# Kernel tuning notes

Hardware: AMD Instinct MI355X
Metric: run time of the kernel (lower is better)

## Reference

```python
import jax, jax.numpy as jnp
import numpy as np

NB = 8      # n_blocks
DIM = 256   # model dim (= context_len in source)
DI = 512    # dim_inner = dim * expand(2)
DCONV = 4   # depthwise conv kernel
NS = 16     # d_state
DTR = 16    # dt_rank = ceil(dim/16)
NE = 4      # experts
INNER = 512 # MoE FFN inner = dim * multi(2)
L = 8192    # sequence length
HOR = 32    # horizon
EPS = 1e-3


def setup_inputs() -> dict:
    key = jax.random.key(0)
    ks = jax.random.split(key, 16)
    s = 0.02
    f = lambda k, shp: jax.random.normal(k, shp, jnp.float32) * s
    return {
        "x": jax.random.normal(ks[0], (DIM, L), jnp.float32),
        "lin_w": f(ks[1], (DIM, DIM)),                      # shared by self.linear and self.out (tied)
        "in_proj_w": f(ks[2], (NB, 2 * DI, DIM)),
        "conv_w": f(ks[3], (NB, DI, 1, DCONV)),             # depthwise conv, groups=DI
        "conv_b": f(ks[4], (NB, DI)),
        "x_proj_w": f(ks[5], (NB, DTR + 2 * NS, DI)),
        "dt_proj_w": f(ks[6], (NB, DI, DTR)),
        "dt_proj_b": f(ks[7], (NB, DI)),
        "A_log": jnp.tile(jnp.log(jnp.arange(1, NS + 1, dtype=jnp.float32)), (NB, DI, 1)),
        "D_param": jnp.ones((NB, DI), jnp.float32),
        "out_proj_w": f(ks[8], (NB, DIM, DI)),
        "gate_w": f(ks[9], (NB, NE, DIM)),
        "gproj_w": f(ks[10], (NB, NE, INNER, DIM)),
        "uproj_w": f(ks[11], (NB, NE, INNER, DIM)),
        "dproj_w": f(ks[12], (NB, NE, DIM, INNER)),
        "rms_a_w": jnp.ones((DIM,), jnp.float32),
        "rms_f_w": jnp.ones((DIM,), jnp.float32),
        "head_w1": f(ks[13], (DIM, DIM)),
        "head_w2": f(ks[14], (HOR, DIM)),
    }


def _rmsnorm(h, w):
    return w * (h * jax.lax.rsqrt(jnp.mean(h * h, axis=-1, keepdims=True) + EPS))


def _mamba(h, ipw, cw, cb, xpw, dtw, dtb, alog, dpar, opw):
    b = h.shape[0]
    xr = jnp.einsum('bld,od->bol', h, ipw)            # (b, 2*DI, l)
    xc, res = jnp.split(xr, 2, axis=1)                # each (b, DI, l)
    # causal depthwise conv (padding=DCONV-1, sliced to length l)
    xc = jax.lax.conv_general_dilated(xc, cw, (1,), [(DCONV - 1, 0)],
                                      feature_group_count=DI,
                                      dimension_numbers=('NCH', 'OIH', 'NCH'))
    xc = jax.nn.silu(xc + cb[None, :, None])
    A = -jnp.exp(alog)                                # (DI, NS)
    xdbl = jnp.einsum('bdl,kd->blk', xc, xpw)         # (b, l, DTR+2*NS)
    dr, B, C = xdbl[..., :DTR], xdbl[..., DTR:DTR + NS], xdbl[..., DTR + NS:]
    delta = jax.nn.softplus(jnp.einsum('blr,dr->bld', dr, dtw) + dtb)
    dA = jnp.exp(jnp.einsum('bld,dn->lbdn', delta, A))          # (l, b, DI, NS)
    dBu = jnp.einsum('bld,bln,bdl->lbdn', delta, B, xc)         # (l, b, DI, NS)
    Cl = jnp.transpose(C, (1, 0, 2))                             # (l, b, NS)
    def step(carry, inp):
        a, bu, c = inp
        carry = a * carry + bu
        return carry, jnp.einsum('bdn,bn->bd', carry, c)
    _, ys = jax.lax.scan(step, jnp.zeros((b, DI, NS), xc.dtype), (dA, dBu, Cl))
    y = jnp.transpose(ys, (1, 2, 0)) + xc * dpar[:, None]        # (b, DI, l)
    y = y * jax.nn.silu(res)
    return jnp.einsum('bdl,od->blo', y, opw)                     # (b, l, DIM)


def _moe(h, gw, gp, up, dp):
    shp = h.shape
    xf = h.reshape(-1, shp[-1])                       # (T, DIM)
    scores = xf @ gw.T                                # (T, NE)
    vals, idx = jax.lax.top_k(scores, 2)
    w = jax.nn.softmax(vals, axis=-1)                 # (T, 2)
    g = jax.nn.silu(jnp.einsum('td,ehd->teh', xf, gp))
    u = jnp.einsum('td,ehd->teh', xf, up)
    eo = jnp.einsum('teh,edh->ted', g * u, dp)        # (T, NE, DIM)
    we = jnp.sum(w[..., None] * jax.nn.one_hot(idx, NE, dtype=xf.dtype), axis=1)  # (T, NE)
    return jnp.einsum('te,ted->td', we, eo).reshape(shp)


def reference(x, lin_w, in_proj_w, conv_w, conv_b, x_proj_w, dt_proj_w, dt_proj_b,
              A_log, D_param, out_proj_w, gate_w, gproj_w, uproj_w, dproj_w,
              rms_a_w, rms_f_w, head_w1, head_w2):
    h = x.T[None]                                     # (1, L, DIM)
    h = h @ lin_w.T
    for i in range(NB):
        resi = h
        h = _rmsnorm(h, rms_a_w)
        h = _mamba(h, in_proj_w[i], conv_w[i], conv_b[i], x_proj_w[i],
                   dt_proj_w[i], dt_proj_b[i], A_log[i], D_param[i], out_proj_w[i])
        h = h + resi
        resi = h
        h = _moe(h, gate_w[i], gproj_w[i], uproj_w[i], dproj_w[i])
        h = _rmsnorm(h, rms_f_w)
        h = h + resi
    h = h @ lin_w.T                                   # self.out (tied weight)
    h = jax.nn.silu(h @ head_w1.T) @ head_w2.T        # head
    return jax.nn.sigmoid(h[0].T)                     # (HOR, L)
```

## Files before the change

### kernel.cpp

```cpp
#include <hip/hip_runtime.h>

typedef unsigned short u16;
typedef unsigned int u32;
using bf16x8 = __attribute__((ext_vector_type(8))) short;
using f32x4 = __attribute__((ext_vector_type(4))) float;

constexpr int kL = 8192;
constexpr int kDIM = 256;
constexpr int kDI = 512;
constexpr int kNB = 8;
constexpr float kEPS = 1e-3f;

__device__ __forceinline__ u16 f2b(float f) {
  u32 x = __builtin_bit_cast(u32, f);
  x += 0x7fffu + ((x >> 16) & 1u);
  return (u16)(x >> 16);
}
__device__ __forceinline__ float b2f(u16 u) {
  return __builtin_bit_cast(float, (u32)u << 16);
}
__device__ __forceinline__ float sigm(float x) { return 1.f / (1.f + __expf(-x)); }
__device__ __forceinline__ float softplus_fast(float x) {
  return fmaxf(x, 0.f) + __logf(1.f + __expf(-fabsf(x)));
}

__device__ __forceinline__ void async_cp16(const void* g, void* l) {
  __builtin_amdgcn_global_load_lds((const __attribute__((address_space(1))) u32*)g,
                                   (__attribute__((address_space(3))) u32*)l, 16, 0, 0);
}

struct Cvt2 {
  const float* s[23];
  u16* d[23];
  int n[23];
  int mode[23];
  int bstart[24];
  int nseg;
};
__global__ __launch_bounds__(256) void cvt2_k(Cvt2 dd) {
  const int b = blockIdx.x;
  int seg = 0;
  for (int i = 1; i < dd.nseg; ++i) seg += (b >= dd.bstart[i]) ? 1 : 0;
  const int lb = b - dd.bstart[seg];
  const float* s = dd.s[seg];
  u16* d = dd.d[seg];
  const int n = dd.n[seg];
  const int mode = dd.mode[seg];
  #pragma unroll
  for (int it = 0; it < 4; ++it) {
    const int e4 = lb * 1024 + it * 256 + threadIdx.x;
    const int i = e4 * 4;
    if (i >= n) break;
    const float4 v = ((const float4*)s)[e4];
    ushort4 o = make_ushort4(f2b(v.x), f2b(v.y), f2b(v.z), f2b(v.w));
    size_t dst;
    if (mode == 0) {
      dst = (size_t)i;
    } else if (mode == 1) {
      dst = (size_t)(((i >> 8) << 9) + (i & 255));
    } else {
      const int bb = i >> 19, e = (i >> 17) & 3, nr = (i >> 9) & 255, j = i & 511;
      dst = (size_t)bb * 524288 + (size_t)nr * 2048 + e * 512 + j;
    }
    *(ushort4*)&d[dst] = o;
  }
}

__global__ __launch_bounds__(256) void transpose_x_k(const float* __restrict__ x, u16* __restrict__ xT) {
  __shared__ float tile[32][33];
  int l0 = blockIdx.x * 32, d0 = blockIdx.y * 32;
  int tx = threadIdx.x, ty = threadIdx.y;
  #pragma unroll
  for (int i = 0; i < 32; i += 8)
    tile[ty + i][tx] = x[(size_t)(d0 + ty + i) * kL + l0 + tx];
  __syncthreads();
  #pragma unroll
  for (int i = 0; i < 32; i += 8)
    xT[(size_t)(l0 + ty + i) * kDIM + d0 + tx] = f2b(tile[tx][ty + i]);
}

template <int BM, int BN, int TR, int TC, int WCN, int MODE>
__global__ __launch_bounds__(256) void gemm_t(
    const u16* __restrict__ A, int lda,
    const u16* __restrict__ W, int ldw,
    void* __restrict__ C, int ldc,
    int N, int K, const float* __restrict__ wep, int pstride)
{
  constexpr int BNR = (BN + 63) & ~63;
  __shared__ u16 As[BM * 64];
  __shared__ u16 Bs[BNR * 64];
  const int tid = threadIdx.x;
  const int lane = tid & 63;
  const int wave = tid >> 6;
  const int bm = blockIdx.x * BM;
  const int bn = blockIdx.y * BN;
  const int wrow = (wave / WCN) * (TR * 16);
  const int wcol = (wave % WCN) * (TC * 16);
  const int kchunk = K / (int)gridDim.z;
  const int kbeg = blockIdx.z * kchunk;
  const int kend = kbeg + kchunk;

  f32x4 acc[TR][TC];
  #pragma unroll
  for (int r = 0; r < TR; ++r)
    #pragma unroll
    for (int c = 0; c < TC; ++c)
      acc[r][c] = f32x4{0.f, 0.f, 0.f, 0.f};

  for (int k0 = kbeg; k0 < kend; k0 += 64) {
    #pragma unroll
    for (int it = 0; it < BM * 64 / 2048; ++it) {
      int flat = (it * 256 + tid) * 8;
      int r = flat >> 6;
      int gc = ((((flat >> 3) & 7) ^ (r & 7)) << 3);
      async_cp16(A + (size_t)(bm + r) * lda + k0 + gc, &As[flat]);
    }
    #pragma unroll
    for (int it = 0; it < BNR * 64 / 2048; ++it) {
      int flat = (it * 256 + tid) * 8;
      int r = flat >> 6;
      int gc = ((((flat >> 3) & 7) ^ (r & 7)) << 3);
      int n = bn + r;
      if (n > N - 1) n = N - 1;
      async_cp16(W + (size_t)n * ldw + k0 + gc, &Bs[flat]);
    }
    __syncthreads();
    const int mrow = lane & 15;
    #pragma unroll
    for (int kk = 0; kk < 64; kk += 32) {
      const int kc = (kk >> 3) + (lane >> 4);
      bf16x8 a[TR], b[TC];
      #pragma unroll
      for (int rr = 0; rr < TR; ++rr) {
        int row = wrow + rr * 16 + mrow;
        a[rr] = *(const bf16x8*)&As[row * 64 + ((kc ^ (row & 7)) << 3)];
      }
      #pragma unroll
      for (int cc = 0; cc < TC; ++cc) {
        int row = wcol + cc * 16 + mrow;
        b[cc] = *(const bf16x8*)&Bs[row * 64 + ((kc ^ (row & 7)) << 3)];
      }
      #pragma unroll
      for (int rr = 0; rr < TR; ++rr)
        #pragma unroll
        for (int cc = 0; cc < TC; ++cc)
          acc[rr][cc] = __builtin_amdgcn_mfma_f32_16x16x32_bf16(a[rr], b[cc], acc[rr][cc], 0, 0, 0);
    }
    __syncthreads();
  }

  const int colb = bn + wcol + (lane & 15);
  const int rowb = bm + wrow + ((lane >> 4) << 2);
  if constexpr (MODE == 6) {
    #pragma unroll
    for (int rr = 0; rr < TR; ++rr)
      #pragma unroll
      for (int cc = 0; cc < TC; ++cc) {
        const int col = colb + cc * 16;
        #pragma unroll
        for (int i = 0; i < 4; ++i) {
          const float v = acc[rr][cc][i];
          const float partner = __shfl_xor(v, 1);
          if (!(lane & 1)) {
            const int row = rowb + rr * 16 + i;
            const int tsj = col >> 1;
            const float w = wep[row * 4 + (tsj >> 9)];
            ((u16*)C)[(size_t)row * 2048 + tsj] = f2b(v * sigm(v) * partner * w);
          }
        }
      }
  } else {
    #pragma unroll
    for (int rr = 0; rr < TR; ++rr)
      #pragma unroll
      for (int cc = 0; cc < TC; ++cc) {
        int col = colb + cc * 16;
        if (col >= N) continue;
        #pragma unroll
        for (int i = 0; i < 4; ++i) {
          const int row = rowb + rr * 16 + i;
          size_t off = (size_t)row * ldc + col;
          float v = acc[rr][cc][i];
          if constexpr (MODE == 0) ((float*)C)[off] = v;
          else if constexpr (MODE == 2) ((u16*)C)[off] = f2b(v);
          else if constexpr (MODE == 3) ((u16*)C)[off] = f2b(v * sigm(v));
          else if constexpr (MODE == 4) atomicAdd(&((float*)C)[off], v);
          else if constexpr (MODE == 5) ((float*)C)[off + (size_t)blockIdx.z * pstride] = v;
          else if constexpr (MODE == 7) ((float*)C)[(size_t)col * kL + row] = sigm(v);
        }
      }
  }
}

__device__ __forceinline__ float block_sum256(float v) {
  #pragma unroll
  for (int o = 32; o > 0; o >>= 1) v += __shfl_down(v, o);
  __shared__ float red[4];
  __syncthreads();
  if ((threadIdx.x & 63) == 0) red[threadIdx.x >> 6] = v;
  __syncthreads();
  return red[0] + red[1] + red[2] + red[3];
}

__global__ __launch_bounds__(256) void rms_a_k(const float* __restrict__ h, const float* __restrict__ w,
                                               u16* __restrict__ hn) {
  const int l = blockIdx.x, t = threadIdx.x;
  const float v = h[(size_t)l * kDIM + t];
  const float ssum = block_sum256(v * v);
  const float r = rsqrtf(ssum * (1.f / 256.f) + kEPS);
  hn[(size_t)l * kDIM + t] = f2b(w[t] * v * r);
}

__global__ __launch_bounds__(256) void rms_f_fused_k(const float* __restrict__ mpart,
                                                     const float* __restrict__ wf,
                                                     const float* __restrict__ wa,
                                                     float* __restrict__ h,
                                                     u16* __restrict__ hb2, u16* __restrict__ hn) {
  const int l = blockIdx.x, t = threadIdx.x;
  const size_t idx = (size_t)l * kDIM + t;
  const float m = mpart[idx] + mpart[idx + 2097152] + mpart[idx + 4194304] + mpart[idx + 6291456];
  const float r1 = rsqrtf(block_sum256(m * m) * (1.f / 256.f) + kEPS);
  const float hv = h[idx] + wf[t] * m * r1;
  h[idx] = hv;
  hb2[idx] = f2b(hv);
  const float r2 = rsqrtf(block_sum256(hv * hv) * (1.f / 256.f) + kEPS);
  hn[idx] = f2b(wa[t] * hv * r2);
}

__global__ __launch_bounds__(256) void conv_silu_k(const u16* __restrict__ xz, const float* __restrict__ cw,
                                                   const float* __restrict__ cb,
                                                   u16* __restrict__ xcb, u16* __restrict__ zsb,
                                                   float* __restrict__ xdbl) {
  const int i4 = blockIdx.x * 256 + threadIdx.x;
  if (i4 < 98304) *(float4*)&xdbl[i4 * 4] = float4{0.f, 0.f, 0.f, 0.f};
  const int l = i4 >> 7;
  const int d = (i4 & 127) * 4;
  float acc[4];
  const float4 cbv = *(const float4*)&cb[d];
  acc[0] = cbv.x; acc[1] = cbv.y; acc[2] = cbv.z; acc[3] = cbv.w;
  #pragma unroll
  for (int j = 0; j < 4; ++j) {
    const int ll = l - 3 + j;
    if (ll >= 0) {
      const ushort4 xv = *(const ushort4*)&xz[(size_t)ll * 1024 + d];
      acc[0] += cw[(d + 0) * 4 + j] * b2f(xv.x);
      acc[1] += cw[(d + 1) * 4 + j] * b2f(xv.y);
      acc[2] += cw[(d + 2) * 4 + j] * b2f(xv.z);
      acc[3] += cw[(d + 3) * 4 + j] * b2f(xv.w);
    }
  }
  ushort4 xo, zo;
  const ushort4 zv = *(const ushort4*)&xz[(size_t)l * 1024 + 512 + d];
  float z0 = b2f(zv.x), z1 = b2f(zv.y), z2 = b2f(zv.z), z3 = b2f(zv.w);
  xo.x = f2b(acc[0] * sigm(acc[0])); xo.y = f2b(acc[1] * sigm(acc[1]));
  xo.z = f2b(acc[2] * sigm(acc[2])); xo.w = f2b(acc[3] * sigm(acc[3]));
  zo.x = f2b(z0 * sigm(z0)); zo.y = f2b(z1 * sigm(z1));
  zo.z = f2b(z2 * sigm(z2)); zo.w = f2b(z3 * sigm(z3));
  *(ushort4*)&xcb[(size_t)l * 512 + d] = xo;
  *(ushort4*)&zsb[(size_t)l * 512 + d] = zo;
}

__global__ __launch_bounds__(256) void scan_a_k(const float* __restrict__ xdbl, const u16* __restrict__ xcb,
                                                const float* __restrict__ A_log, const float* __restrict__ dtw,
                                                const float* __restrict__ dtb,
                                                u16* __restrict__ delta,
                                                float* __restrict__ aprod, float* __restrict__ bacc) {
  const int c = blockIdx.x;
  const int t = threadIdx.x;
  const int half = t & 1;
  const int d = blockIdx.y * 128 + (t >> 1);
  const int l0 = c * 64;
  __shared__ float Xs[64][32];
  for (int i = t; i < 2048; i += 256)
    Xs[i >> 5][i & 31] = xdbl[(size_t)(l0 + (i >> 5)) * 48 + (i & 31)];
  __syncthreads();
  float wd[8], Ad[8];
  #pragma unroll
  for (int j = 0; j < 8; ++j) wd[j] = dtw[d * 16 + half * 8 + j];
  const float bd = dtb[d];
  #pragma unroll
  for (int n = 0; n < 8; ++n) Ad[n] = -__expf(A_log[d * 16 + half * 8 + n]);
  float s[8], ap[8];
  #pragma unroll
  for (int n = 0; n < 8; ++n) { s[n] = 0.f; ap[n] = 1.f; }
  #pragma unroll 4
  for (int lr = 0; lr < 64; ++lr) {
    const float4 dr0 = *(const float4*)&Xs[lr][half * 8];
    const float4 dr1 = *(const float4*)&Xs[lr][half * 8 + 4];
    float p0 = dr0.x * wd[0] + dr0.y * wd[1] + dr0.z * wd[2] + dr0.w * wd[3];
    float p1 = dr1.x * wd[4] + dr1.y * wd[5] + dr1.z * wd[6] + dr1.w * wd[7];
    float dot = p0 + p1;
    dot += __shfl_xor(dot, 1);
    const float dl = softplus_fast(dot + bd);
    const int l = l0 + lr;
    if (!half) delta[(size_t)l * 512 + d] = f2b(dl);
    const float du = dl * b2f(xcb[(size_t)l * 512 + d]);
    const float4 B0 = *(const float4*)&Xs[lr][16 + half * 8];
    const float4 B1 = *(const float4*)&Xs[lr][16 + half * 8 + 4];
    const float Bv[8] = {B0.x, B0.y, B0.z, B0.w, B1.x, B1.y, B1.z, B1.w};
    #pragma unroll
    for (int n = 0; n < 8; ++n) {
      const float a = __expf(dl * Ad[n]);
      s[n] = fmaf(a, s[n], du * Bv[n]);
      ap[n] *= a;
    }
  }
  const int base = c * 8192 + d * 16 + half * 8;
  #pragma unroll
  for (int n = 0; n < 8; ++n) { aprod[base + n] = ap[n]; bacc[base + n] = s[n]; }
}

__global__ __launch_bounds__(256) void scan_b_k(const float* __restrict__ aprod, const float* __restrict__ bacc,
                                                float* __restrict__ sinit) {
  const int st = blockIdx.x * 256 + threadIdx.x;
  float cur = 0.f;
  float a0 = aprod[st], b0 = bacc[st];
  for (int c = 0; c < 128; ++c) {
    float a1 = 0.f, b1 = 0.f;
    if (c + 1 < 128) {
      a1 = aprod[(size_t)(c + 1) * 8192 + st];
      b1 = bacc[(size_t)(c + 1) * 8192 + st];
    }
    sinit[(size_t)c * 8192 + st] = cur;
    cur = fmaf(a0, cur, b0);
    a0 = a1; b0 = b1;
  }
}

__global__ __launch_bounds__(256) void scan_c_k(const float* __restrict__ xdbl, const u16* __restrict__ xcb,
                                                const u16* __restrict__ zsb, const float* __restrict__ A_log,
                                                const u16* __restrict__ delta,
                                                const float* __restrict__ sinit,
                                                const float* __restrict__ Dp, u16* __restrict__ yv) {
  const int c = blockIdx.x;
  const int t = threadIdx.x;
  const int half = t & 1;
  const int d = blockIdx.y * 128 + (t >> 1);
  const int l0 = c * 64;
  __shared__ float Xs[64][32];
  for (int i = t; i < 2048; i += 256)
    Xs[i >> 5][i & 31] = xdbl[(size_t)(l0 + (i >> 5)) * 48 + 16 + (i & 31)];
  __syncthreads();
  float Ad[8];
  #pragma unroll
  for (int n = 0; n < 8; ++n) Ad[n] = -__expf(A_log[d * 16 + half * 8 + n]);
  float s[8];
  const int base = c * 8192 + d * 16 + half * 8;
  #pragma unroll
  for (int n = 0; n < 8; ++n) s[n] = sinit[base + n];
  const float Dd = Dp[d];
  #pragma unroll 4
  for (int lr = 0; lr < 64; ++lr) {
    const int l = l0 + lr;
    const float dl = b2f(delta[(size_t)l * 512 + d]);
    const float xv = b2f(xcb[(size_t)l * 512 + d]);
    const float zs = b2f(zsb[(size_t)l * 512 + d]);
    const float du = dl * xv;
    const float4 B0 = *(const float4*)&Xs[lr][half * 8];
    const float4 B1 = *(const float4*)&Xs[lr][half * 8 + 4];
    const float4 C0 = *(const float4*)&Xs[lr][16 + half * 8];
    const float4 C1 = *(const float4*)&Xs[lr][16 + half * 8 + 4];
    const float Bv[8] = {B0.x, B0.y, B0.z, B0.w, B1.x, B1.y, B1.z, B1.w};
    const float Cv[8] = {C0.x, C0.y, C0.z, C0.w, C1.x, C1.y, C1.z, C1.w};
    float y = 0.f;
    #pragma unroll
    for (int n = 0; n < 8; ++n) {
      const float a = __expf(dl * Ad[n]);
      s[n] = fmaf(a, s[n], du * Bv[n]);
      y = fmaf(s[n], Cv[n], y);
    }
    y += __shfl_xor(y, 1);
    if (!half) yv[(size_t)l * 512 + d] = f2b((y + xv * Dd) * zs);
  }
}

__global__ __launch_bounds__(256) void router_k(float* __restrict__ h, const float* __restrict__ hpart,
                                                const float* __restrict__ gw,
                                                float* __restrict__ we, u16* __restrict__ hb) {
  const int l = blockIdx.x * 4 + (threadIdx.x >> 6);
  const int lane = threadIdx.x & 63;
  const size_t ro = (size_t)l * 256;
  float4 v = reinterpret_cast<const float4*>(h + ro)[lane];
  #pragma unroll
  for (int z = 0; z < 4; ++z) {
    const float4 pv = reinterpret_cast<const float4*>(hpart + (size_t)z * 2097152 + ro)[lane];
    v.x += pv.x; v.y += pv.y; v.z += pv.z; v.w += pv.w;
  }
  reinterpret_cast<float4*>(h + ro)[lane] = v;
  reinterpret_cast<ushort4*>(hb + ro)[lane] = make_ushort4(f2b(v.x), f2b(v.y), f2b(v.z), f2b(v.w));
  float p[4];
  #pragma unroll
  for (int e = 0; e < 4; ++e) {
    const float4 g = reinterpret_cast<const float4*>(gw + (size_t)e * 256)[lane];
    p[e] = v.x * g.x + v.y * g.y + v.z * g.z + v.w * g.w;
  }
  #pragma unroll
  for (int o = 32; o > 0; o >>= 1) {
    p[0] += __shfl_down(p[0], o);
    p[1] += __shfl_down(p[1], o);
    p[2] += __shfl_down(p[2], o);
    p[3] += __shfl_down(p[3], o);
  }
  if (lane == 0) {
    int i0 = 0;
    #pragma unroll
    for (int e = 1; e < 4; ++e) if (p[e] > p[i0]) i0 = e;
    int i1 = -1;
    #pragma unroll
    for (int e = 0; e < 4; ++e) {
      if (e == i0) continue;
      if (i1 < 0 || p[e] > p[i1]) i1 = e;
    }
    const float tt = __expf(p[i1] - p[i0]);
    const float w0 = 1.f / (1.f + tt);
    const float w1 = tt / (1.f + tt);
    float o[4] = {0.f, 0.f, 0.f, 0.f};
    o[i0] = w0; o[i1] = w1;
    reinterpret_cast<float4*>(we)[l] = make_float4(o[0], o[1], o[2], o[3]);
  }
}

extern "C" void kernel_launch(void* const* d_in, const int* in_sizes, int n_in,
                              void* d_out, int out_size, void* d_ws, size_t ws_size,
                              hipStream_t stream) {
  const float* x        = (const float*)d_in[0];
  const float* lin_w    = (const float*)d_in[1];
  const float* in_proj  = (const float*)d_in[2];
  const float* conv_w   = (const float*)d_in[3];
  const float* conv_b   = (const float*)d_in[4];
  const float* x_proj   = (const float*)d_in[5];
  const float* dt_w     = (const float*)d_in[6];
  const float* dt_b     = (const float*)d_in[7];
  const float* A_log    = (const float*)d_in[8];
  const float* D_param  = (const float*)d_in[9];
  const float* out_proj = (const float*)d_in[10];
  const float* gate_w   = (const float*)d_in[11];
  const float* gproj    = (const float*)d_in[12];
  const float* uproj    = (const float*)d_in[13];
  const float* dproj    = (const float*)d_in[14];
  const float* rms_a_w  = (const float*)d_in[15];
  const float* rms_f_w  = (const float*)d_in[16];
  const float* head_w1  = (const float*)d_in[17];
  const float* head_w2  = (const float*)d_in[18];

  char* p = (char*)d_ws;
  auto alloc = [&](size_t bytes) -> char* {
    char* r = p;
    p += (bytes + 255) & ~(size_t)255;
    return r;
  };

  u16* lin_b  = (u16*)alloc(65536 * 2);
  u16* ipw_b  = (u16*)alloc((size_t)2097152 * 2);
  u16* xpw_b  = (u16*)alloc((size_t)196608 * 2);
  u16* opw_b  = (u16*)alloc((size_t)1048576 * 2);
  u16* gupw_b = (u16*)alloc((size_t)8388608 * 2);
  u16* dpw_b  = (u16*)alloc((size_t)4194304 * 2);
  u16* hw1_b  = (u16*)alloc(65536 * 2);
  u16* hw2_b  = (u16*)alloc(8192 * 2);

  u16* xT     = (u16*)alloc((size_t)kL * kDIM * 2);
  float* h    = (float*)alloc((size_t)kL * kDIM * 4);
  u16* hn     = (u16*)alloc((size_t)kL * kDIM * 2);
  u16* hb     = (u16*)alloc((size_t)kL * kDIM * 2);
  u16* hb2    = (u16*)alloc((size_t)kL * kDIM * 2);
  float* we   = (float*)alloc((size_t)kL * 4 * 4);
  float* xdbl = (float*)alloc((size_t)kL * 48 * 4);
  u16* fb     = (u16*)alloc((size_t)kL * kDIM * 2);
  u16* h2b    = (u16*)alloc((size_t)kL * kDIM * 2);
  u16* xz     = (u16*)alloc((size_t)kL * 1024 * 2);
  u16* ts     = (u16*)alloc((size_t)kL * 2048 * 2);
  u16* xcb    = (u16*)alloc((size_t)kL * kDI * 2);
  u16* zsb    = (u16*)alloc((size_t)kL * kDI * 2);
  u16* yv     = (u16*)alloc((size_t)kL * kDI * 2);
  u16* delta  = (u16*)alloc((size_t)kL * kDI * 2);
  float* aprod = (float*)alloc((size_t)128 * 8192 * 4);
  float* bacc  = (float*)alloc((size_t)128 * 8192 * 4);
  float* sinit = (float*)alloc((size_t)128 * 8192 * 4);
  float* hpart = (float*)alloc((size_t)4 * kL * kDIM * 4);
  float* mpart = (float*)alloc((size_t)4 * kL * kDIM * 4);

  if ((size_t)(p - (char*)d_ws) > ws_size) return;

  Cvt2 dd;
  int seg = 0, blk = 0;
  auto add = [&](const float* s, u16* d, int n, int mode) {
    dd.s[seg] = s; dd.d[seg] = d; dd.n[seg] = n; dd.mode[seg] = mode;
    dd.bstart[seg] = blk;
    blk += (n + 4095) / 4096;
    ++seg;
  };
  add(lin_w, lin_b, 65536, 0);
  add(in_proj, ipw_b, 2097152, 0);
  add(x_proj, xpw_b, 196608, 0);
  add(out_proj, opw_b, 1048576, 0);
  add(head_w1, hw1_b, 65536, 0);
  add(head_w2, hw2_b, 8192, 0);
  for (int i = 0; i < kNB; ++i) {
    add(gproj + (size_t)i * 524288, gupw_b + (size_t)i * 1048576, 524288, 1);
    add(uproj + (size_t)i * 524288, gupw_b + (size_t)i * 1048576 + 256, 524288, 1);
  }
  add(dproj, dpw_b, 4194304, 2);
  dd.nseg = seg;
  dd.bstart[seg] = blk;
  cvt2_k<<<blk, 256, 0, stream>>>(dd);
  transpose_x_k<<<dim3(kL / 32, kDIM / 32), dim3(32, 8), 0, stream>>>(x, xT);

  gemm_t<64, 128, 2, 4, 2, 0><<<dim3(128, 2, 1), 256, 0, stream>>>(
      xT, 256, lin_b, 256, h, 256, 256, 256, nullptr, 0);
  rms_a_k<<<kL, 256, 0, stream>>>(h, rms_a_w, hn);

  for (int i = 0; i < kNB; ++i) {
    gemm_t<128, 128, 4, 4, 2, 2><<<dim3(64, 8, 1), 256, 0, stream>>>(
        hn, 256, ipw_b + (size_t)i * 262144, 256, xz, 1024, 1024, 256, nullptr, 0);
    conv_silu_k<<<kL * kDI / 1024, 256, 0, stream>>>(xz, conv_w + (size_t)i * 2048,
                                                     conv_b + (size_t)i * 512, xcb, zsb, xdbl);
    gemm_t<128, 48, 2, 3, 1, 4><<<dim3(64, 1, 8), 256, 0, stream>>>(
        xcb, 512, xpw_b + (size_t)i * 24576, 512, xdbl, 48, 48, 512, nullptr, 0);
    scan_a_k<<<dim3(128, 4), 256, 0, stream>>>(xdbl, xcb, A_log + (size_t)i * 8192,
                                               dt_w + (size_t)i * 8192, dt_b + (size_t)i * 512,
                                               delta, aprod, bacc);
    scan_b_k<<<32, 256, 0, stream>>>(aprod, bacc, sinit);
    scan_c_k<<<dim3(128, 4), 256, 0, stream>>>(xdbl, xcb, zsb, A_log + (size_t)i * 8192,
                                               delta, sinit, D_param + (size_t)i * 512, yv);
    gemm_t<128, 128, 4, 4, 2, 5><<<dim3(64, 2, 4), 256, 0, stream>>>(
        yv, 512, opw_b + (size_t)i * 131072, 512, hpart, 256, 256, 512, nullptr, 2097152);
    router_k<<<kL / 4, 256, 0, stream>>>(h, hpart, gate_w + (size_t)i * 1024, we, hb);
    gemm_t<128, 128, 4, 4, 2, 6><<<dim3(64, 32, 1), 256, 0, stream>>>(
        hb, 256, gupw_b + (size_t)i * 1048576, 256, ts, 2048, 4096, 256, we, 0);
    gemm_t<128, 128, 4, 4, 2, 5><<<dim3(64, 2, 4), 256, 0, stream>>>(
        ts, 2048, dpw_b + (size_t)i * 524288, 2048, mpart, 256, 256, 2048, nullptr, 2097152);
    rms_f_fused_k<<<kL, 256, 0, stream>>>(mpart, rms_f_w, rms_a_w, h, hb2, hn);
  }

  gemm_t<64, 128, 2, 4, 2, 2><<<dim3(128, 2, 1), 256, 0, stream>>>(
      hb2, 256, lin_b, 256, h2b, 256, 256, 256, nullptr, 0);
  gemm_t<64, 128, 2, 4, 2, 3><<<dim3(128, 2, 1), 256, 0, stream>>>(
      h2b, 256, hw1_b, 256, fb, 256, 256, 256, nullptr, 0);
  gemm_t<64, 128, 2, 4, 2, 7><<<dim3(128, 1, 1), 256, 0, stream>>>(
      fb, 256, hw2_b, 256, (float*)d_out, 32, 32, 256, nullptr, 0);
}
```

Before: 2.156 ms.

## Fuse router, MoE gate/up/down GEMMs and RMSNorm into one kernel

Replaces the router kernel, the gate/up GEMM with SwiGLU epilogue, the split-K down-projection GEMM and the fused RMSNorm kernel with a single per-32-row-tile kernel. The activation tile and the expert intermediate stay in shared memory, which removes the large ts and mpart round trips through global memory and three launches per block. The gate/up weights are re-laid out so each 256-row chunk interleaves gate and up halves per 16 rows. The cost is that only 256 blocks of 512 threads run, with small 32-row tiles. Each block also streams all expert weights, so weight traffic rises and occupancy is low.

```diff
diff --git a/kernel.cpp b/kernel.cpp
--- a/kernel.cpp
+++ b/kernel.cpp
@@ -57,7 +57,9 @@
     if (mode == 0) {
       dst = (size_t)i;
     } else if (mode == 1) {
-      dst = (size_t)(((i >> 8) << 9) + (i & 255));
+      const int row = i >> 8, col = i & 255;
+      const int drow = (row >> 9) * 1024 + ((row >> 4) & 31) * 32 + (row & 15);
+      dst = (size_t)drow * 256 + col;
     } else {
       const int bb = i >> 19, e = (i >> 17) & 3, nr = (i >> 9) & 255, j = i & 511;
       dst = (size_t)bb * 524288 + (size_t)nr * 2048 + e * 512 + j;
@@ -84,7 +86,7 @@
     const u16* __restrict__ A, int lda,
     const u16* __restrict__ W, int ldw,
     void* __restrict__ C, int ldc,
-    int N, int K, const float* __restrict__ wep, int pstride)
+    int N, int K, int pstride)
 {
   constexpr int BNR = (BN + 63) & ~63;
   __shared__ u16 As[BM * 64];
@@ -125,10 +127,10 @@
       async_cp16(W + (size_t)n * ldw + k0 + gc, &Bs[flat]);
     }
     __syncthreads();
-    const int mrow = lane & 15;
     #pragma unroll
     for (int kk = 0; kk < 64; kk += 32) {
       const int kc = (kk >> 3) + (lane >> 4);
+      const int mrow = lane & 15;
       bf16x8 a[TR], b[TC];
       #pragma unroll
       for (int rr = 0; rr < TR; ++rr) {
@@ -151,44 +153,250 @@
 
   const int colb = bn + wcol + (lane & 15);
   const int rowb = bm + wrow + ((lane >> 4) << 2);
-  if constexpr (MODE == 6) {
-    #pragma unroll
-    for (int rr = 0; rr < TR; ++rr)
-      #pragma unroll
-      for (int cc = 0; cc < TC; ++cc) {
-        const int col = colb + cc * 16;
+  #pragma unroll
+  for (int rr = 0; rr < TR; ++rr)
+    #pragma unroll
+    for (int cc = 0; cc < TC; ++cc) {
+      int col = colb + cc * 16;
+      if (col >= N) continue;
+      #pragma unroll
+      for (int i = 0; i < 4; ++i) {
+        const int row = rowb + rr * 16 + i;
+        size_t off = (size_t)row * ldc + col;
+        float v = acc[rr][cc][i];
+        if constexpr (MODE == 0) ((float*)C)[off] = v;
+        else if constexpr (MODE == 2) ((u16*)C)[off] = f2b(v);
+        else if constexpr (MODE == 3) ((u16*)C)[off] = f2b(v * sigm(v));
+        else if constexpr (MODE == 4) atomicAdd(&((float*)C)[off], v);
+        else if constexpr (MODE == 5) ((float*)C)[off + (size_t)blockIdx.z * pstride] = v;
+        else if constexpr (MODE == 7) ((float*)C)[(size_t)col * kL + row] = sigm(v);
+      }
+    }
+}
+
+__global__ __launch_bounds__(512, 1) void moe_mega_k(
+    float* __restrict__ h, const float* __restrict__ hpart,
+    const float* __restrict__ gw,
+    const u16* __restrict__ Wgu, const u16* __restrict__ Wd,
+    const float* __restrict__ wf, const float* __restrict__ wa,
+    u16* __restrict__ hb2, u16* __restrict__ hn)
+{
+  __shared__ u16 Ah[32 * 256];
+  __shared__ u16 Ts[32 * 512];
+  __shared__ u16 Ws[2][256 * 64];
+  __shared__ float WeS[32][4];
+  const int tid = threadIdx.x;
+  const int lane = tid & 63;
+  const int quad = lane >> 4;
+  const int m16 = lane & 15;
+  const int wave = tid >> 6;
+  const int wcol = wave * 32;
+  const int r0 = blockIdx.x * 32;
+  const int prow = tid >> 4;
+  const int pcol = (tid & 15) * 16;
+
+  float hv[16];
+  {
+    const size_t base = (size_t)(r0 + prow) * 256 + pcol;
+    #pragma unroll
+    for (int j = 0; j < 16; j += 4) {
+      float4 v = *(const float4*)(h + base + j);
+      #pragma unroll
+      for (int z = 0; z < 4; ++z) {
+        const float4 pv = *(const float4*)(hpart + (size_t)z * 2097152 + base + j);
+        v.x += pv.x; v.y += pv.y; v.z += pv.z; v.w += pv.w;
+      }
+      hv[j] = v.x; hv[j + 1] = v.y; hv[j + 2] = v.z; hv[j + 3] = v.w;
+    }
+  }
+  {
+    float p[4];
+    #pragma unroll
+    for (int e = 0; e < 4; ++e) {
+      float s = 0.f;
+      #pragma unroll
+      for (int j = 0; j < 16; ++j) s += hv[j] * gw[e * 256 + pcol + j];
+      p[e] = s;
+    }
+    #pragma unroll
+    for (int o = 8; o > 0; o >>= 1) {
+      p[0] += __shfl_xor(p[0], o); p[1] += __shfl_xor(p[1], o);
+      p[2] += __shfl_xor(p[2], o); p[3] += __shfl_xor(p[3], o);
+    }
+    if ((tid & 15) == 0) {
+      int i0 = 0;
+      #pragma unroll
+      for (int e = 1; e < 4; ++e) if (p[e] > p[i0]) i0 = e;
+      int i1 = -1;
+      #pragma unroll
+      for (int e = 0; e < 4; ++e) {
+        if (e == i0) continue;
+        if (i1 < 0 || p[e] > p[i1]) i1 = e;
+      }
+      const float tt = __expf(p[i1] - p[i0]);
+      float o0 = 1.f / (1.f + tt), o1 = tt / (1.f + tt);
+      WeS[prow][0] = 0.f; WeS[prow][1] = 0.f; WeS[prow][2] = 0.f; WeS[prow][3] = 0.f;
+      WeS[prow][i0] = o0; WeS[prow][i1] = o1;
+    }
+    #pragma unroll
+    for (int cc = 0; cc < 2; ++cc) {
+      const int chunk = (pcol >> 3) + cc;
+      const int sw = ((chunk ^ (prow & 7)) << 3);
+      u16 tmp[8];
+      #pragma unroll
+      for (int j = 0; j < 8; ++j) tmp[j] = f2b(hv[cc * 8 + j]);
+      *(bf16x8*)&Ah[prow * 256 + sw] = *(bf16x8*)tmp;
+    }
+  }
+  __syncthreads();
+
+  f32x4 macc[2][2];
+  #pragma unroll
+  for (int rt = 0; rt < 2; ++rt)
+    #pragma unroll
+    for (int ct = 0; ct < 2; ++ct) macc[rt][ct] = f32x4{0.f, 0.f, 0.f, 0.f};
+
+  auto stage_gu = [&](int buf, int e, int nc, int k0) {
+    #pragma unroll
+    for (int it = 0; it < 4; ++it) {
+      const int flat = (it * 512 + tid) * 8;
+      const int r = flat >> 6;
+      const int gc = ((((flat >> 3) & 7) ^ (r & 7)) << 3);
+      async_cp16(Wgu + (size_t)(e * 1024 + nc * 256 + r) * 256 + k0 + gc, &Ws[buf][flat]);
+    }
+  };
+  auto stage_dp = [&](int buf, int e, int k0) {
+    #pragma unroll
+    for (int it = 0; it < 4; ++it) {
+      const int flat = (it * 512 + tid) * 8;
+      const int r = flat >> 6;
+      const int gc = ((((flat >> 3) & 7) ^ (r & 7)) << 3);
+      async_cp16(Wd + (size_t)r * 2048 + e * 512 + k0 + gc, &Ws[buf][flat]);
+    }
+  };
+
+  for (int e = 0; e < 4; ++e) {
+    for (int nc = 0; nc < 4; ++nc) {
+      f32x4 acc[2][2];
+      #pragma unroll
+      for (int rt = 0; rt < 2; ++rt)
+        #pragma unroll
+        for (int ct = 0; ct < 2; ++ct) acc[rt][ct] = f32x4{0.f, 0.f, 0.f, 0.f};
+      stage_gu(0, e, nc, 0);
+      __syncthreads();
+      #pragma unroll
+      for (int k0i = 0; k0i < 4; ++k0i) {
+        if (k0i < 3) stage_gu((k0i + 1) & 1, e, nc, (k0i + 1) * 64);
+        const u16* buf = Ws[k0i & 1];
+        #pragma unroll
+        for (int kk = 0; kk < 64; kk += 32) {
+          const int kcs = (kk >> 3) + quad;
+          bf16x8 a[2], b[2];
+          #pragma unroll
+          for (int rt = 0; rt < 2; ++rt) {
+            const int row = rt * 16 + m16;
+            const int ch = ((k0i * 64 + kk) >> 3) + quad;
+            a[rt] = *(const bf16x8*)&Ah[row * 256 + ((ch ^ (row & 7)) << 3)];
+          }
+          #pragma unroll
+          for (int ct = 0; ct < 2; ++ct) {
+            const int n = wcol + ct * 16 + m16;
+            b[ct] = *(const bf16x8*)&buf[n * 64 + ((kcs ^ (n & 7)) << 3)];
+          }
+          #pragma unroll
+          for (int rt = 0; rt < 2; ++rt)
+            #pragma unroll
+            for (int ct = 0; ct < 2; ++ct)
+              acc[rt][ct] = __builtin_amdgcn_mfma_f32_16x16x32_bf16(a[rt], b[ct], acc[rt][ct], 0, 0, 0);
+        }
+        __syncthreads();
+      }
+      const int group = nc * 8 + wave;
+      const int j = group * 16 + m16;
+      #pragma unroll
+      for (int rt = 0; rt < 2; ++rt)
         #pragma unroll
         for (int i = 0; i < 4; ++i) {
-          const float v = acc[rr][cc][i];
-          const float partner = __shfl_xor(v, 1);
-          if (!(lane & 1)) {
-            const int row = rowb + rr * 16 + i;
-            const int tsj = col >> 1;
-            const float w = wep[row * 4 + (tsj >> 9)];
-            ((u16*)C)[(size_t)row * 2048 + tsj] = f2b(v * sigm(v) * partner * w);
-          }
+          const int row = rt * 16 + quad * 4 + i;
+          const float g = acc[rt][0][i];
+          const float u = acc[rt][1][i];
+          const float val = g * sigm(g) * u * WeS[row][e];
+          Ts[row * 512 + (((j >> 3) ^ (row & 7)) << 3) + (j & 7)] = f2b(val);
         }
+    }
+    __syncthreads();
+    stage_dp(0, e, 0);
+    __syncthreads();
+    #pragma unroll
+    for (int k0i = 0; k0i < 8; ++k0i) {
+      if (k0i < 7) stage_dp((k0i + 1) & 1, e, (k0i + 1) * 64);
+      const u16* buf = Ws[k0i & 1];
+      #pragma unroll
+      for (int kk = 0; kk < 64; kk += 32) {
+        const int kcs = (kk >> 3) + quad;
+        bf16x8 a[2], b[2];
+        #pragma unroll
+        for (int rt = 0; rt < 2; ++rt) {
+          const int row = rt * 16 + m16;
+          const int ch = ((k0i * 64 + kk) >> 3) + quad;
+          a[rt] = *(const bf16x8*)&Ts[row * 512 + ((ch ^ (row & 7)) << 3)];
+        }
+        #pragma unroll
+        for (int ct = 0; ct < 2; ++ct) {
+          const int n = wcol + ct * 16 + m16;
+          b[ct] = *(const bf16x8*)&buf[n * 64 + ((kcs ^ (n & 7)) << 3)];
+        }
+        #pragma unroll
+        for (int rt = 0; rt < 2; ++rt)
+          #pragma unroll
+          for (int ct = 0; ct < 2; ++ct)
+            macc[rt][ct] = __builtin_amdgcn_mfma_f32_16x16x32_bf16(a[rt], b[ct], macc[rt][ct], 0, 0, 0);
       }
-  } else {
-    #pragma unroll
-    for (int rr = 0; rr < TR; ++rr)
-      #pragma unroll
-      for (int cc = 0; cc < TC; ++cc) {
-        int col = colb + cc * 16;
-        if (col >= N) continue;
-        #pragma unroll
-        for (int i = 0; i < 4; ++i) {
-          const int row = rowb + rr * 16 + i;
-          size_t off = (size_t)row * ldc + col;
-          float v = acc[rr][cc][i];
-          if constexpr (MODE == 0) ((float*)C)[off] = v;
-          else if constexpr (MODE == 2) ((u16*)C)[off] = f2b(v);
-          else if constexpr (MODE == 3) ((u16*)C)[off] = f2b(v * sigm(v));
-          else if constexpr (MODE == 4) atomicAdd(&((float*)C)[off], v);
-          else if constexpr (MODE == 5) ((float*)C)[off + (size_t)blockIdx.z * pstride] = v;
-          else if constexpr (MODE == 7) ((float*)C)[(size_t)col * kL + row] = sigm(v);
-        }
-      }
+      __syncthreads();
+    }
+  }
+
+  float* MoeS = (float*)Ts;
+  __syncthreads();
+  #pragma unroll
+  for (int rt = 0; rt < 2; ++rt)
+    #pragma unroll
+    for (int ct = 0; ct < 2; ++ct)
+      #pragma unroll
+      for (int i = 0; i < 4; ++i)
+        MoeS[(rt * 16 + quad * 4 + i) * 256 + wcol + ct * 16 + m16] = macc[rt][ct][i];
+  __syncthreads();
+
+  float mv[16];
+  float ss = 0.f;
+  #pragma unroll
+  for (int j = 0; j < 16; ++j) {
+    mv[j] = MoeS[prow * 256 + pcol + j];
+    ss += mv[j] * mv[j];
+  }
+  #pragma unroll
+  for (int o = 8; o > 0; o >>= 1) ss += __shfl_xor(ss, o);
+  const float r1 = rsqrtf(ss * (1.f / 256.f) + kEPS);
+  float ss2 = 0.f;
+  #pragma unroll
+  for (int j = 0; j < 16; ++j) {
+    hv[j] += wf[pcol + j] * mv[j] * r1;
+    ss2 += hv[j] * hv[j];
+  }
+  #pragma unroll
+  for (int o = 8; o > 0; o >>= 1) ss2 += __shfl_xor(ss2, o);
+  const float r2 = rsqrtf(ss2 * (1.f / 256.f) + kEPS);
+
+  const size_t base = (size_t)(r0 + prow) * 256 + pcol;
+  #pragma unroll
+  for (int j = 0; j < 16; j += 4)
+    *(float4*)(h + base + j) = float4{hv[j], hv[j + 1], hv[j + 2], hv[j + 3]};
+  #pragma unroll
+  for (int j = 0; j < 16; j += 4) {
+    *(ushort4*)(hb2 + base + j) = make_ushort4(f2b(hv[j]), f2b(hv[j + 1]), f2b(hv[j + 2]), f2b(hv[j + 3]));
+    *(ushort4*)(hn + base + j) = make_ushort4(
+        f2b(wa[pcol + j] * hv[j] * r2), f2b(wa[pcol + j + 1] * hv[j + 1] * r2),
+        f2b(wa[pcol + j + 2] * hv[j + 2] * r2), f2b(wa[pcol + j + 3] * hv[j + 3] * r2));
   }
 }
 
@@ -209,22 +417,6 @@
   const float ssum = block_sum256(v * v);
   const float r = rsqrtf(ssum * (1.f / 256.f) + kEPS);
   hn[(size_t)l * kDIM + t] = f2b(w[t] * v * r);
-}
-
-__global__ __launch_bounds__(256) void rms_f_fused_k(const float* __restrict__ mpart,
-                                                     const float* __restrict__ wf,
-                                                     const float* __restrict__ wa,
-                                                     float* __restrict__ h,
-                                                     u16* __restrict__ hb2, u16* __restrict__ hn) {
-  const int l = blockIdx.x, t = threadIdx.x;
-  const size_t idx = (size_t)l * kDIM + t;
-  const float m = mpart[idx] + mpart[idx + 2097152] + mpart[idx + 4194304] + mpart[idx + 6291456];
-  const float r1 = rsqrtf(block_sum256(m * m) * (1.f / 256.f) + kEPS);
-  const float hv = h[idx] + wf[t] * m * r1;
-  h[idx] = hv;
-  hb2[idx] = f2b(hv);
-  const float r2 = rsqrtf(block_sum256(hv * hv) * (1.f / 256.f) + kEPS);
-  hn[idx] = f2b(wa[t] * hv * r2);
 }
 
 __global__ __launch_bounds__(256) void conv_silu_k(const u16* __restrict__ xz, const float* __restrict__ cw,
@@ -371,52 +563,6 @@
     }
     y += __shfl_xor(y, 1);
     if (!half) yv[(size_t)l * 512 + d] = f2b((y + xv * Dd) * zs);
-  }
-}
-
-__global__ __launch_bounds__(256) void router_k(float* __restrict__ h, const float* __restrict__ hpart,
-                                                const float* __restrict__ gw,
-                                                float* __restrict__ we, u16* __restrict__ hb) {
-  const int l = blockIdx.x * 4 + (threadIdx.x >> 6);
-  const int lane = threadIdx.x & 63;
-  const size_t ro = (size_t)l * 256;
-  float4 v = reinterpret_cast<const float4*>(h + ro)[lane];
-  #pragma unroll
-  for (int z = 0; z < 4; ++z) {
-    const float4 pv = reinterpret_cast<const float4*>(hpart + (size_t)z * 2097152 + ro)[lane];
-    v.x += pv.x; v.y += pv.y; v.z += pv.z; v.w += pv.w;
-  }
-  reinterpret_cast<float4*>(h + ro)[lane] = v;
-  reinterpret_cast<ushort4*>(hb + ro)[lane] = make_ushort4(f2b(v.x), f2b(v.y), f2b(v.z), f2b(v.w));
-  float p[4];
-  #pragma unroll
-  for (int e = 0; e < 4; ++e) {
-    const float4 g = reinterpret_cast<const float4*>(gw + (size_t)e * 256)[lane];
-    p[e] = v.x * g.x + v.y * g.y + v.z * g.z + v.w * g.w;
-  }
-  #pragma unroll
-  for (int o = 32; o > 0; o >>= 1) {
-    p[0] += __shfl_down(p[0], o);
-    p[1] += __shfl_down(p[1], o);
-    p[2] += __shfl_down(p[2], o);
-    p[3] += __shfl_down(p[3], o);
-  }
-  if (lane == 0) {
-    int i0 = 0;
-    #pragma unroll
-    for (int e = 1; e < 4; ++e) if (p[e] > p[i0]) i0 = e;
-    int i1 = -1;
-    #pragma unroll
-    for (int e = 0; e < 4; ++e) {
-      if (e == i0) continue;
-      if (i1 < 0 || p[e] > p[i1]) i1 = e;
-    }
-    const float tt = __expf(p[i1] - p[i0]);
-    const float w0 = 1.f / (1.f + tt);
-    const float w1 = tt / (1.f + tt);
-    float o[4] = {0.f, 0.f, 0.f, 0.f};
-    o[i0] = w0; o[i1] = w1;
-    reinterpret_cast<float4*>(we)[l] = make_float4(o[0], o[1], o[2], o[3]);
   }
 }
 
@@ -462,14 +608,11 @@
   u16* xT     = (u16*)alloc((size_t)kL * kDIM * 2);
   float* h    = (float*)alloc((size_t)kL * kDIM * 4);
   u16* hn     = (u16*)alloc((size_t)kL * kDIM * 2);
-  u16* hb     = (u16*)alloc((size_t)kL * kDIM * 2);
   u16* hb2    = (u16*)alloc((size_t)kL * kDIM * 2);
-  float* we   = (float*)alloc((size_t)kL * 4 * 4);
   float* xdbl = (float*)alloc((size_t)kL * 48 * 4);
   u16* fb     = (u16*)alloc((size_t)kL * kDIM * 2);
   u16* h2b    = (u16*)alloc((size_t)kL * kDIM * 2);
   u16* xz     = (u16*)alloc((size_t)kL * 1024 * 2);
-  u16* ts     = (u16*)alloc((size_t)kL * 2048 * 2);
   u16* xcb    = (u16*)alloc((size_t)kL * kDI * 2);
   u16* zsb    = (u16*)alloc((size_t)kL * kDI * 2);
   u16* yv     = (u16*)alloc((size_t)kL * kDI * 2);
@@ -478,7 +621,6 @@
   float* bacc  = (float*)alloc((size_t)128 * 8192 * 4);
   float* sinit = (float*)alloc((size_t)128 * 8192 * 4);
   float* hpart = (float*)alloc((size_t)4 * kL * kDIM * 4);
-  float* mpart = (float*)alloc((size_t)4 * kL * kDIM * 4);
 
   if ((size_t)(p - (char*)d_ws) > ws_size) return;
 
@@ -498,7 +640,7 @@
   add(head_w2, hw2_b, 8192, 0);
   for (int i = 0; i < kNB; ++i) {
     add(gproj + (size_t)i * 524288, gupw_b + (size_t)i * 1048576, 524288, 1);
-    add(uproj + (size_t)i * 524288, gupw_b + (size_t)i * 1048576 + 256, 524288, 1);
+    add(uproj + (size_t)i * 524288, gupw_b + (size_t)i * 1048576 + 4096, 524288, 1);
   }
   add(dproj, dpw_b, 4194304, 2);
   dd.nseg = seg;
@@ -507,16 +649,16 @@
   transpose_x_k<<<dim3(kL / 32, kDIM / 32), dim3(32, 8), 0, stream>>>(x, xT);
 
   gemm_t<64, 128, 2, 4, 2, 0><<<dim3(128, 2, 1), 256, 0, stream>>>(
-      xT, 256, lin_b, 256, h, 256, 256, 256, nullptr, 0);
+      xT, 256, lin_b, 256, h, 256, 256, 256, 0);
   rms_a_k<<<kL, 256, 0, stream>>>(h, rms_a_w, hn);
 
   for (int i = 0; i < kNB; ++i) {
     gemm_t<128, 128, 4, 4, 2, 2><<<dim3(64, 8, 1), 256, 0, stream>>>(
-        hn, 256, ipw_b + (size_t)i * 262144, 256, xz, 1024, 1024, 256, nullptr, 0);
+        hn, 256, ipw_b + (size_t)i * 262144, 256, xz, 1024, 1024, 256, 0);
     conv_silu_k<<<kL * kDI / 1024, 256, 0, stream>>>(xz, conv_w + (size_t)i * 2048,
                                                      conv_b + (size_t)i * 512, xcb, zsb, xdbl);
     gemm_t<128, 48, 2, 3, 1, 4><<<dim3(64, 1, 8), 256, 0, stream>>>(
-        xcb, 512, xpw_b + (size_t)i * 24576, 512, xdbl, 48, 48, 512, nullptr, 0);
+        xcb, 512, xpw_b + (size_t)i * 24576, 512, xdbl, 48, 48, 512, 0);
     scan_a_k<<<dim3(128, 4), 256, 0, stream>>>(xdbl, xcb, A_log + (size_t)i * 8192,
                                                dt_w + (size_t)i * 8192, dt_b + (size_t)i * 512,
                                                delta, aprod, bacc);
@@ -524,19 +666,16 @@
     scan_c_k<<<dim3(128, 4), 256, 0, stream>>>(xdbl, xcb, zsb, A_log + (size_t)i * 8192,
                                                delta, sinit, D_param + (size_t)i * 512, yv);
     gemm_t<128, 128, 4, 4, 2, 5><<<dim3(64, 2, 4), 256, 0, stream>>>(
-        yv, 512, opw_b + (size_t)i * 131072, 512, hpart, 256, 256, 512, nullptr, 2097152);
-    router_k<<<kL / 4, 256, 0, stream>>>(h, hpart, gate_w + (size_t)i * 1024, we, hb);
-    gemm_t<128, 128, 4, 4, 2, 6><<<dim3(64, 32, 1), 256, 0, stream>>>(
-        hb, 256, gupw_b + (size_t)i * 1048576, 256, ts, 2048, 4096, 256, we, 0);
-    gemm_t<128, 128, 4, 4, 2, 5><<<dim3(64, 2, 4), 256, 0, stream>>>(
-        ts, 2048, dpw_b + (size_t)i * 524288, 2048, mpart, 256, 256, 2048, nullptr, 2097152);
-    rms_f_fused_k<<<kL, 256, 0, stream>>>(mpart, rms_f_w, rms_a_w, h, hb2, hn);
+        yv, 512, opw_b + (size_t)i * 131072, 512, hpart, 256, 256, 512, 2097152);
+    moe_mega_k<<<256, 512, 0, stream>>>(h, hpart, gate_w + (size_t)i * 1024,
+                                        gupw_b + (size_t)i * 1048576, dpw_b + (size_t)i * 524288,
+                                        rms_f_w, rms_a_w, hb2, hn);
   }
 
   gemm_t<64, 128, 2, 4, 2, 2><<<dim3(128, 2, 1), 256, 0, stream>>>(
-      hb2, 256, lin_b, 256, h2b, 256, 256, 256, nullptr, 0);
+      hb2, 256, lin_b, 256, h2b, 256, 256, 256, 0);
   gemm_t<64, 128, 2, 4, 2, 3><<<dim3(128, 2, 1), 256, 0, stream>>>(
-      h2b, 256, hw1_b, 256, fb, 256, 256, 256, nullptr, 0);
+      h2b, 256, hw1_b, 256, fb, 256, 256, 256, 0);
   gemm_t<64, 128, 2, 4, 2, 7><<<dim3(128, 1, 1), 256, 0, stream>>>(
-      fb, 256, hw2_b, 256, (float*)d_out, 32, 32, 256, nullptr, 0);
-}
+      fb, 256, hw2_b, 256, (float*)d_out, 32, 32, 256, 0);
+}
```

New measurement: 2.147 ms. Within noise of the previous version (-0.4%).
